# Kernel tuning notes

Measured on AMD Instinct MI355X. Metric: run time of the kernel, lower is better.

Reference implementation:

```python
import jax, jax.numpy as jnp
import numpy as np

DIM, WIDTH = 5, 64
BATCH, N_SAVE = 4096, 64
RTOL, ATOL = 1e-3, 1e-6
SAFETY, FMIN, FMAX = 0.9, 0.2, 10.0
MAX_STEPS, DT0, EPS = 64, 0.1, 1e-6

# Tsit5 (Tsitouras 2011) Butcher tableau
A21 = 0.161
A31, A32 = -0.008480655492356989, 0.335480655492357
A41, A42, A43 = 2.8971530571054935, -6.359448489975075, 4.3622954328695815
A51, A52, A53, A54 = 5.325864828439257, -11.748883564062828, 7.4955393428898365, -0.09249506636175525
A61, A62, A63, A64, A65 = 5.86145544294642, -12.92096931784711, 8.159367898576159, -0.071584973281401, -0.028269050394068383
B1, B2, B3, B4, B5, B6 = 0.09646076681806523, 0.01, 0.4798896504144996, 1.379008574103742, -3.290069515436081, 2.324710524099774
# embedded 4th-order error coefficients (b - bhat)
E1, E2, E3, E4, E5, E6, E7 = (-0.00178001105222577714, -0.0008164344596567469,
    0.007880878010261995, -0.1447110071732629, 0.5823571654525552,
    -0.45808210592918697, 0.015151515151515152)


def _mlp(y, W1, b1, W2, b2, W3, b3, W4, b4):
    # eqx.nn.MLP(5, 5, width 64, depth 3, softplus)
    h = jax.nn.softplus(y @ W1.T + b1)
    h = jax.nn.softplus(h @ W2.T + b2)
    h = jax.nn.softplus(h @ W3.T + b3)
    return h @ W4.T + b4


def _solve_one(y0, t_eval, params):
    f = lambda y: _mlp(y, *params)
    t0, t1 = t_eval[0], t_eval[-1]
    # save points at/before t0 get y0
    ys0 = jnp.where((t_eval <= t0 + EPS)[:, None], y0[None, :], 0.0)

    def body(carry, _):
        t, y, h, ys = carry
        done = t >= t1 - EPS
        hc = jnp.where(done, 0.0, jnp.minimum(h, t1 - t))  # clip last step to t1
        k1 = f(y)
        k2 = f(y + hc * (A21 * k1))
        k3 = f(y + hc * (A31 * k1 + A32 * k2))
        k4 = f(y + hc * (A41 * k1 + A42 * k2 + A43 * k3))
        k5 = f(y + hc * (A51 * k1 + A52 * k2 + A53 * k3 + A54 * k4))
        k6 = f(y + hc * (A61 * k1 + A62 * k2 + A63 * k3 + A64 * k4 + A65 * k5))
        ynew = y + hc * (B1 * k1 + B2 * k2 + B3 * k3 + B4 * k4 + B5 * k5 + B6 * k6)
        k7 = f(ynew)  # FSAL stage, also used for error + interpolation
        err = hc * (E1 * k1 + E2 * k2 + E3 * k3 + E4 * k4 + E5 * k5 + E6 * k6 + E7 * k7)
        scale = ATOL + RTOL * jnp.maximum(jnp.abs(y), jnp.abs(ynew))
        enorm = jnp.sqrt(jnp.mean((err / scale) ** 2))
        enorm_c = jax.lax.stop_gradient(jnp.maximum(enorm, 1e-10))
        accept = enorm <= 1.0
        factor = jnp.clip(SAFETY * enorm_c ** -0.2, FMIN, FMAX)  # I-controller, order 5
        step_ok = accept & ~done
        t_next = jnp.where(step_ok, t + hc, t)
        y_next = jnp.where(step_ok, ynew, y)
        h_next = jnp.where(done, h, hc * factor)
        # cubic Hermite interpolation for save points inside (t, t_next]
        s = ((t_eval - t) / jnp.maximum(hc, 1e-12))[:, None]
        h00 = 2 * s**3 - 3 * s**2 + 1
        h10 = s**3 - 2 * s**2 + s
        h01 = -2 * s**3 + 3 * s**2
        h11 = s**3 - s**2
        yi = h00 * y + h10 * hc * k1 + h01 * ynew + h11 * hc * k7
        mask = (t_eval > t) & (t_eval <= t_next + EPS) & step_ok
        ys = jnp.where(mask[:, None], yi, ys)
        return (t_next, y_next, h_next, ys), None

    h0 = jnp.asarray(DT0, dtype=y0.dtype)
    (_, _, _, ys), _ = jax.lax.scan(body, (t0, y0, h0, ys0), None, length=MAX_STEPS)
    return ys  # [N_SAVE, DIM]


def setup_inputs() -> dict:
    key = jax.random.key(0)
    ks = jax.random.split(key, 9)
    y0 = jax.random.normal(ks[0], (BATCH, DIM), dtype=jnp.float32)
    t_eval = jnp.linspace(0.0, 1.0, N_SAVE, dtype=jnp.float32)

    def lin(k, out_d, in_d):
        lim = 1.0 / np.sqrt(in_d)
        kw, kb = jax.random.split(k)
        W = jax.random.uniform(kw, (out_d, in_d), jnp.float32, -lim, lim)
        b = jax.random.uniform(kb, (out_d,), jnp.float32, -lim, lim)
        return W, b

    W1, b1 = lin(ks[1], WIDTH, DIM)
    W2, b2 = lin(ks[2], WIDTH, WIDTH)
    W3, b3 = lin(ks[3], WIDTH, WIDTH)
    W4, b4 = lin(ks[4], DIM, WIDTH)
    return {"y0": y0, "t_eval": t_eval, "W1": W1, "b1": b1, "W2": W2, "b2": b2,
            "W3": W3, "b3": b3, "W4": W4, "b4": b4}


def reference(y0, t_eval, W1, b1, W2, b2, W3, b3, W4, b4):
    params = (W1, b1, W2, b2, W3, b3, W4, b4)
    return jax.vmap(lambda y: _solve_one(y, t_eval, params))(y0)  # [BATCH, N_SAVE, DIM]
```

## Files before the change

kernel.cpp:

```cpp
#include <hip/hip_runtime.h>
#include <cmath>

namespace {

constexpr int kDim = 5;
constexpr int kSave = 64;
constexpr int kTraj = 16;
constexpr int kThreads = 256;
constexpr int kMaxSteps = 64;
constexpr int HS = 72;
constexpr int SD = 8;

typedef _Float16 half8 __attribute__((ext_vector_type(8)));
typedef float f32x4 __attribute__((ext_vector_type(4)));

__device__ __forceinline__ float softplusf(float x) {
  return fmaxf(x, 0.0f) + __logf(1.0f + __expf(-fabsf(x)));
}

__global__ __launch_bounds__(kThreads, 1)
void node_tsit5_kernel(const float* __restrict__ gy0,
                       const float* __restrict__ gte,
                       const float* __restrict__ gW1, const float* __restrict__ gb1,
                       const float* __restrict__ gW2, const float* __restrict__ gb2,
                       const float* __restrict__ gW3, const float* __restrict__ gb3,
                       const float* __restrict__ gW4, const float* __restrict__ gb4,
                       float* __restrict__ out) {
  const float A21 = 0.161f;
  const float A31 = -0.008480655492356989f, A32 = 0.335480655492357f;
  const float A41 = 2.8971530571054935f, A42 = -6.359448489975075f, A43 = 4.3622954328695815f;
  const float A51 = 5.325864828439257f, A52 = -11.748883564062828f, A53 = 7.4955393428898365f,
              A54 = -0.09249506636175525f;
  const float A61 = 5.86145544294642f, A62 = -12.92096931784711f, A63 = 8.159367898576159f,
              A64 = -0.071584973281401f, A65 = -0.028269050394068383f;
  const float B1 = 0.09646076681806523f, B2 = 0.01f, B3 = 0.4798896504144996f,
              B4 = 1.379008574103742f, B5 = -3.290069515436081f, B6 = 2.324710524099774f;
  const float E1 = -0.00178001105222577714f, E2 = -0.0008164344596567469f,
              E3 = 0.007880878010261995f, E4 = -0.1447110071732629f, E5 = 0.5823571654525552f,
              E6 = -0.45808210592918697f, E7 = 0.015151515151515152f;

  __shared__ __align__(16) _Float16 h0[kTraj * HS], l0[kTraj * HS];
  __shared__ __align__(16) _Float16 h1[kTraj * HS], l1[kTraj * HS];
  __shared__ __align__(16) _Float16 h2[kTraj * HS], l2[kTraj * HS];
  __shared__ float sTe[kSave];
  __shared__ float sY[kTraj * SD], sYN[kTraj * SD], sK1[kTraj * SD], sK7[kTraj * SD];
  __shared__ float ctT[kTraj], ctH[kTraj], ctN[kTraj], ctO[kTraj];

  const int tid = threadIdx.x;
  const int bid = blockIdx.x;
  const int w = tid >> 6;
  const int ln = tid & 63;
  const int quad = ln >> 4;
  const int col = ln & 15;
  const int row0 = quad * 4;
  const int nn = (w << 4) | col;
  const bool cact = col < kDim;
  const bool w0 = (w == 0);

  half8 w2h[2], w3h[2], w4h[2], mfh[2];
  float w1r[kDim];
  #pragma unroll
  for (int d = 0; d < kDim; ++d) w1r[d] = gW1[nn * 5 + d];
  #pragma unroll
  for (int kf = 0; kf < 2; ++kf)
    #pragma unroll
    for (int j = 0; j < 8; ++j) {
      int kk2 = kf * 32 + quad * 8 + j;
      w2h[kf][j] = (_Float16)gW2[nn * 64 + kk2];
      w3h[kf][j] = (_Float16)gW3[nn * 64 + kk2];
      w4h[kf][j] = cact ? (_Float16)gW4[col * 64 + kk2] : (_Float16)0.0f;
      float m = 0.0f;
      #pragma unroll
      for (int d = 0; d < kDim; ++d) m = fmaf(w1r[d], gW4[d * 64 + kk2], m);
      mfh[kf][j] = (_Float16)m;
    }
  const float c1 = gb1[nn], c2 = gb2[nn], c3 = gb3[nn];
  const float c4 = cact ? gb4[col] : 0.0f;
  float cu = 0.0f;
  #pragma unroll
  for (int d = 0; d < kDim; ++d) cu = fmaf(w1r[d], gb4[d], cu);

  if (tid < kSave) sTe[tid] = gte[tid];
  if (tid < kTraj * kDim) {
    int t = tid & 15, d = tid >> 4;
    sY[t * SD + d] = gy0[(size_t)(bid * kTraj + t) * kDim + d];
  }
  {
    float* ob = out + (size_t)bid * kTraj * kSave * kDim;
    for (int idx = tid; idx < kTraj * kSave * kDim; idx += kThreads) ob[idx] = 0.0f;
  }

  f32x4 syr = {0, 0, 0, 0}, synr = {0, 0, 0, 0}, kk[7], uu[7], p_y;
  #pragma unroll
  for (int r = 0; r < 4; ++r) {
    const float* yr = gy0 + (size_t)(bid * kTraj + row0 + r) * kDim;
    float acc = c1;
    #pragma unroll
    for (int d = 0; d < kDim; ++d) acc = fmaf(w1r[d], yr[d], acc);
    p_y[r] = acc;
    if (cact) syr[r] = yr[col];
  }
  __syncthreads();

  const float t0v = sTe[0];
  const float t1v = sTe[kSave - 1];

  {
    int tt = tid & 15, gg = tid >> 4;
    float yv[kDim];
    #pragma unroll
    for (int d = 0; d < kDim; ++d) yv[d] = sY[tt * SD + d];
    #pragma unroll
    for (int q = 0; q < 4; ++q) {
      int n = 4 * gg + q;
      if (sTe[n] <= t0v + 1e-6f) {
        float* op = out + ((size_t)(bid * kTraj + tt) * kSave + n) * kDim;
        #pragma unroll
        for (int d = 0; d < kDim; ++d) op[d] = yv[d];
      }
    }
  }

  auto evalF = [&](f32x4 pre1, f32x4& kOut, f32x4& uOut) {
    #pragma unroll
    for (int r = 0; r < 4; ++r) {
      float s = softplusf(pre1[r]);
      _Float16 hi = (_Float16)s;
      h0[(row0 + r) * HS + nn] = hi;
      l0[(row0 + r) * HS + nn] = (_Float16)(s - (float)hi);
    }
    __syncthreads();
    {
      half8 ah0 = *(const half8*)(h0 + col * HS + quad * 8);
      half8 ah1 = *(const half8*)(h0 + col * HS + 32 + quad * 8);
      half8 al0 = *(const half8*)(l0 + col * HS + quad * 8);
      half8 al1 = *(const half8*)(l0 + col * HS + 32 + quad * 8);
      f32x4 a = {c2, c2, c2, c2};
      f32x4 b = {0, 0, 0, 0};
      a = __builtin_amdgcn_mfma_f32_16x16x32_f16(ah0, w2h[0], a, 0, 0, 0);
      b = __builtin_amdgcn_mfma_f32_16x16x32_f16(al0, w2h[0], b, 0, 0, 0);
      a = __builtin_amdgcn_mfma_f32_16x16x32_f16(ah1, w2h[1], a, 0, 0, 0);
      b = __builtin_amdgcn_mfma_f32_16x16x32_f16(al1, w2h[1], b, 0, 0, 0);
      a += b;
      #pragma unroll
      for (int r = 0; r < 4; ++r) {
        float s = softplusf(a[r]);
        _Float16 hi = (_Float16)s;
        h1[(row0 + r) * HS + nn] = hi;
        l1[(row0 + r) * HS + nn] = (_Float16)(s - (float)hi);
      }
    }
    __syncthreads();
    {
      half8 ah0 = *(const half8*)(h1 + col * HS + quad * 8);
      half8 ah1 = *(const half8*)(h1 + col * HS + 32 + quad * 8);
      half8 al0 = *(const half8*)(l1 + col * HS + quad * 8);
      half8 al1 = *(const half8*)(l1 + col * HS + 32 + quad * 8);
      f32x4 a = {c3, c3, c3, c3};
      f32x4 b = {0, 0, 0, 0};
      a = __builtin_amdgcn_mfma_f32_16x16x32_f16(ah0, w3h[0], a, 0, 0, 0);
      b = __builtin_amdgcn_mfma_f32_16x16x32_f16(al0, w3h[0], b, 0, 0, 0);
      a = __builtin_amdgcn_mfma_f32_16x16x32_f16(ah1, w3h[1], a, 0, 0, 0);
      b = __builtin_amdgcn_mfma_f32_16x16x32_f16(al1, w3h[1], b, 0, 0, 0);
      a += b;
      #pragma unroll
      for (int r = 0; r < 4; ++r) {
        float s = softplusf(a[r]);
        _Float16 hi = (_Float16)s;
        h2[(row0 + r) * HS + nn] = hi;
        l2[(row0 + r) * HS + nn] = (_Float16)(s - (float)hi);
      }
    }
    __syncthreads();
    {
      half8 ah0 = *(const half8*)(h2 + col * HS + quad * 8);
      half8 ah1 = *(const half8*)(h2 + col * HS + 32 + quad * 8);
      half8 al0 = *(const half8*)(l2 + col * HS + quad * 8);
      half8 al1 = *(const half8*)(l2 + col * HS + 32 + quad * 8);
      f32x4 ka = {c4, c4, c4, c4};
      f32x4 kb = {0, 0, 0, 0};
      f32x4 ua = {cu, cu, cu, cu};
      f32x4 ub = {0, 0, 0, 0};
      ka = __builtin_amdgcn_mfma_f32_16x16x32_f16(ah0, w4h[0], ka, 0, 0, 0);
      kb = __builtin_amdgcn_mfma_f32_16x16x32_f16(al0, w4h[0], kb, 0, 0, 0);
      ua = __builtin_amdgcn_mfma_f32_16x16x32_f16(ah0, mfh[0], ua, 0, 0, 0);
      ub = __builtin_amdgcn_mfma_f32_16x16x32_f16(al0, mfh[0], ub, 0, 0, 0);
      ka = __builtin_amdgcn_mfma_f32_16x16x32_f16(ah1, w4h[1], ka, 0, 0, 0);
      kb = __builtin_amdgcn_mfma_f32_16x16x32_f16(al1, w4h[1], kb, 0, 0, 0);
      ua = __builtin_amdgcn_mfma_f32_16x16x32_f16(ah1, mfh[1], ua, 0, 0, 0);
      ub = __builtin_amdgcn_mfma_f32_16x16x32_f16(al1, mfh[1], ub, 0, 0, 0);
      kOut = ka + kb;
      uOut = ua + ub;
    }
  };

  evalF(p_y, kk[0], uu[0]);

  f32x4 tcur = {t0v, t0v, t0v, t0v};
  f32x4 hcur = {0.1f, 0.1f, 0.1f, 0.1f};

  for (int step = 0; step < kMaxSteps; ++step) {
    f32x4 hcs, tOldr;
    bool dnr[4];
    bool all4 = true;
    #pragma unroll
    for (int r = 0; r < 4; ++r) {
      bool d = tcur[r] >= t1v - 1e-6f;
      dnr[r] = d;
      all4 &= d;
      hcs[r] = d ? 0.0f : fminf(hcur[r], t1v - tcur[r]);
      tOldr[r] = tcur[r];
    }
    if (__ballot(all4) == ~0ull) break;

    f32x4 p1;
    #pragma unroll
    for (int r = 0; r < 4; ++r) p1[r] = fmaf(hcs[r], A21 * uu[0][r], p_y[r]);
    evalF(p1, kk[1], uu[1]);

    #pragma unroll
    for (int r = 0; r < 4; ++r)
      p1[r] = fmaf(hcs[r], fmaf(A32, uu[1][r], A31 * uu[0][r]), p_y[r]);
    evalF(p1, kk[2], uu[2]);

    #pragma unroll
    for (int r = 0; r < 4; ++r)
      p1[r] = fmaf(hcs[r], fmaf(A43, uu[2][r], fmaf(A42, uu[1][r], A41 * uu[0][r])), p_y[r]);
    evalF(p1, kk[3], uu[3]);

    #pragma unroll
    for (int r = 0; r < 4; ++r)
      p1[r] = fmaf(hcs[r], fmaf(A54, uu[3][r], fmaf(A53, uu[2][r],
                  fmaf(A52, uu[1][r], A51 * uu[0][r]))), p_y[r]);
    evalF(p1, kk[4], uu[4]);

    #pragma unroll
    for (int r = 0; r < 4; ++r)
      p1[r] = fmaf(hcs[r], fmaf(A65, uu[4][r], fmaf(A64, uu[3][r], fmaf(A63, uu[2][r],
                  fmaf(A62, uu[1][r], A61 * uu[0][r])))), p_y[r]);
    evalF(p1, kk[5], uu[5]);

    f32x4 bu;
    #pragma unroll
    for (int r = 0; r < 4; ++r) {
      bu[r] = fmaf(B6, uu[5][r], fmaf(B5, uu[4][r], fmaf(B4, uu[3][r],
              fmaf(B3, uu[2][r], fmaf(B2, uu[1][r], B1 * uu[0][r])))));
      synr[r] = fmaf(hcs[r], fmaf(B6, kk[5][r], fmaf(B5, kk[4][r], fmaf(B4, kk[3][r],
                 fmaf(B3, kk[2][r], fmaf(B2, kk[1][r], B1 * kk[0][r]))))), syr[r]);
      p1[r] = fmaf(hcs[r], bu[r], p_y[r]);
    }
    if (w0 && cact) {
      #pragma unroll
      for (int r = 0; r < 4; ++r) {
        int o = (row0 + r) * SD + col;
        sY[o] = syr[r];
        sYN[o] = synr[r];
        sK1[o] = kk[0][r];
      }
    }
    evalF(p1, kk[6], uu[6]);

    f32x4 rr2;
    #pragma unroll
    for (int r = 0; r < 4; ++r) {
      float err = hcs[r] * fmaf(E7, kk[6][r], fmaf(E6, kk[5][r], fmaf(E5, kk[4][r],
                  fmaf(E4, kk[3][r], fmaf(E3, kk[2][r], fmaf(E2, kk[1][r], E1 * kk[0][r]))))));
      float sc = fmaf(1e-3f, fmaxf(fabsf(syr[r]), fabsf(synr[r])), 1e-6f);
      float rr = err / sc;
      rr2[r] = cact ? rr * rr : 0.0f;
    }
    #pragma unroll
    for (int m = 1; m < 16; m <<= 1) {
      #pragma unroll
      for (int r = 0; r < 4; ++r) rr2[r] += __shfl_xor(rr2[r], m, 64);
    }

    bool okr[4];
    #pragma unroll
    for (int r = 0; r < 4; ++r) {
      float enorm = sqrtf(rr2[r] / 5.0f);
      float enc = fmaxf(enorm, 1e-10f);
      bool accept = enorm <= 1.0f;
      float factor = fminf(fmaxf(0.9f * __expf(-0.2f * __logf(enc)), 0.2f), 10.0f);
      bool ok = accept && !dnr[r];
      okr[r] = ok;
      tcur[r] = ok ? tcur[r] + hcs[r] : tcur[r];
      hcur[r] = dnr[r] ? hcur[r] : hcs[r] * factor;
    }

    if (w0 && cact) {
      #pragma unroll
      for (int r = 0; r < 4; ++r) sK7[(row0 + r) * SD + col] = kk[6][r];
    }
    if (w0 && col == 0) {
      #pragma unroll
      for (int r = 0; r < 4; ++r) {
        int m2 = row0 + r;
        ctT[m2] = tOldr[r];
        ctH[m2] = hcs[r];
        ctN[m2] = tcur[r];
        ctO[m2] = okr[r] ? 1.0f : 0.0f;
      }
    }
    __syncthreads();

    {
      int tt = tid & 15, gg = tid >> 4;
      if (ctO[tt] != 0.0f) {
        float tOld = ctT[tt], hcv = ctH[tt], tNew = ctN[tt];
        float inv = 1.0f / fmaxf(hcv, 1e-12f);
        float yv[kDim], ynv[kDim], k1v[kDim], k7v[kDim];
        #pragma unroll
        for (int d = 0; d < kDim; ++d) {
          yv[d] = sY[tt * SD + d];
          ynv[d] = sYN[tt * SD + d];
          k1v[d] = hcv * sK1[tt * SD + d];
          k7v[d] = hcv * sK7[tt * SD + d];
        }
        #pragma unroll
        for (int q = 0; q < 4; ++q) {
          int n = 4 * gg + q;
          float te = sTe[n];
          if (te > tOld && te <= tNew + 1e-6f) {
            float sx = (te - tOld) * inv;
            float s2 = sx * sx, s3 = s2 * sx;
            float h00 = 2.f * s3 - 3.f * s2 + 1.f;
            float h10 = s3 - 2.f * s2 + sx;
            float h01 = -2.f * s3 + 3.f * s2;
            float h11 = s3 - s2;
            float* op = out + ((size_t)(bid * kTraj + tt) * kSave + n) * kDim;
            #pragma unroll
            for (int d = 0; d < kDim; ++d)
              op[d] = h00 * yv[d] + h10 * k1v[d] + h01 * ynv[d] + h11 * k7v[d];
          }
        }
      }
    }

    #pragma unroll
    for (int r = 0; r < 4; ++r) {
      if (okr[r]) {
        syr[r] = synr[r];
        kk[0][r] = kk[6][r];
        uu[0][r] = uu[6][r];
        p_y[r] = fmaf(hcs[r], bu[r], p_y[r]);
      }
    }
  }
}

}

extern "C" void kernel_launch(void* const* d_in, const int* in_sizes, int n_in,
                              void* d_out, int out_size, void* d_ws, size_t ws_size,
                              hipStream_t stream) {
  const float* y0 = (const float*)d_in[0];
  const float* te = (const float*)d_in[1];
  const float* W1 = (const float*)d_in[2];
  const float* b1 = (const float*)d_in[3];
  const float* W2 = (const float*)d_in[4];
  const float* b2 = (const float*)d_in[5];
  const float* W3 = (const float*)d_in[6];
  const float* b3 = (const float*)d_in[7];
  const float* W4 = (const float*)d_in[8];
  const float* b4 = (const float*)d_in[9];
  float* out = (float*)d_out;

  const int batch = in_sizes[0] / kDim;
  const int blocks = batch / kTraj;
  hipLaunchKernelGGL(node_tsit5_kernel, dim3(blocks), dim3(kThreads), 0, stream,
                     y0, te, W1, b1, W2, b2, W3, b3, W4, b4, out);
}
```

Measured before the change: 107.8 us.

## Process two interleaved trajectory groups per block to amortize barriers

Each block now integrates two independent groups of 16 trajectories, running the MLP layers for both groups between each shared barrier. Launching half as many blocks means each __syncthreads and its latency is shared by twice the MFMA and softplus work, which gives more independent instructions to overlap. In exchange, register and shared-memory use per block roughly doubles. Fewer blocks (128) may underfill the GPU's compute units, and the early-exit check now waits for the slower of both groups.

```diff
diff --git a/kernel.cpp b/kernel.cpp
--- a/kernel.cpp
+++ b/kernel.cpp
@@ -6,6 +6,7 @@
 constexpr int kDim = 5;
 constexpr int kSave = 64;
 constexpr int kTraj = 16;
+constexpr int kStreams = 2;
 constexpr int kThreads = 256;
 constexpr int kMaxSteps = 64;
 constexpr int HS = 72;
@@ -39,12 +40,14 @@
               E3 = 0.007880878010261995f, E4 = -0.1447110071732629f, E5 = 0.5823571654525552f,
               E6 = -0.45808210592918697f, E7 = 0.015151515151515152f;
 
-  __shared__ __align__(16) _Float16 h0[kTraj * HS], l0[kTraj * HS];
-  __shared__ __align__(16) _Float16 h1[kTraj * HS], l1[kTraj * HS];
-  __shared__ __align__(16) _Float16 h2[kTraj * HS], l2[kTraj * HS];
+  __shared__ __align__(16) _Float16 h0[kStreams][kTraj * HS], l0[kStreams][kTraj * HS];
+  __shared__ __align__(16) _Float16 h1[kStreams][kTraj * HS], l1[kStreams][kTraj * HS];
+  __shared__ __align__(16) _Float16 h2[kStreams][kTraj * HS], l2[kStreams][kTraj * HS];
   __shared__ float sTe[kSave];
-  __shared__ float sY[kTraj * SD], sYN[kTraj * SD], sK1[kTraj * SD], sK7[kTraj * SD];
-  __shared__ float ctT[kTraj], ctH[kTraj], ctN[kTraj], ctO[kTraj];
+  __shared__ float sY[kStreams][kTraj * SD], sYN[kStreams][kTraj * SD];
+  __shared__ float sK1[kStreams][kTraj * SD], sK7[kStreams][kTraj * SD];
+  __shared__ float ctT[kStreams][kTraj], ctH[kStreams][kTraj];
+  __shared__ float ctN[kStreams][kTraj], ctO[kStreams][kTraj];
 
   const int tid = threadIdx.x;
   const int bid = blockIdx.x;
@@ -81,24 +84,30 @@
   for (int d = 0; d < kDim; ++d) cu = fmaf(w1r[d], gb4[d], cu);
 
   if (tid < kSave) sTe[tid] = gte[tid];
-  if (tid < kTraj * kDim) {
-    int t = tid & 15, d = tid >> 4;
-    sY[t * SD + d] = gy0[(size_t)(bid * kTraj + t) * kDim + d];
+  if (tid < kStreams * kTraj * kDim) {
+    int s = tid / (kTraj * kDim), rem = tid % (kTraj * kDim);
+    int t = rem & 15, d = rem >> 4;
+    sY[s][t * SD + d] = gy0[(size_t)(bid * kStreams * kTraj + s * kTraj + t) * kDim + d];
   }
   {
-    float* ob = out + (size_t)bid * kTraj * kSave * kDim;
-    for (int idx = tid; idx < kTraj * kSave * kDim; idx += kThreads) ob[idx] = 0.0f;
-  }
-
-  f32x4 syr = {0, 0, 0, 0}, synr = {0, 0, 0, 0}, kk[7], uu[7], p_y;
+    float* ob = out + (size_t)bid * kStreams * kTraj * kSave * kDim;
+    for (int idx = tid; idx < kStreams * kTraj * kSave * kDim; idx += kThreads)
+      ob[idx] = 0.0f;
+  }
+
+  f32x4 syr[kStreams], synr[kStreams], kkS[kStreams][7], uuS[kStreams][7], p_y[kStreams];
   #pragma unroll
-  for (int r = 0; r < 4; ++r) {
-    const float* yr = gy0 + (size_t)(bid * kTraj + row0 + r) * kDim;
-    float acc = c1;
-    #pragma unroll
-    for (int d = 0; d < kDim; ++d) acc = fmaf(w1r[d], yr[d], acc);
-    p_y[r] = acc;
-    if (cact) syr[r] = yr[col];
+  for (int s = 0; s < kStreams; ++s) {
+    syr[s] = f32x4{0, 0, 0, 0};
+    #pragma unroll
+    for (int r = 0; r < 4; ++r) {
+      const float* yr = gy0 + (size_t)(bid * kStreams * kTraj + s * kTraj + row0 + r) * kDim;
+      float acc = c1;
+      #pragma unroll
+      for (int d = 0; d < kDim; ++d) acc = fmaf(w1r[d], yr[d], acc);
+      p_y[s][r] = acc;
+      if (cact) syr[s][r] = yr[col];
+    }
   }
   __syncthreads();
 
@@ -107,34 +116,42 @@
 
   {
     int tt = tid & 15, gg = tid >> 4;
-    float yv[kDim];
-    #pragma unroll
-    for (int d = 0; d < kDim; ++d) yv[d] = sY[tt * SD + d];
-    #pragma unroll
-    for (int q = 0; q < 4; ++q) {
-      int n = 4 * gg + q;
-      if (sTe[n] <= t0v + 1e-6f) {
-        float* op = out + ((size_t)(bid * kTraj + tt) * kSave + n) * kDim;
-        #pragma unroll
-        for (int d = 0; d < kDim; ++d) op[d] = yv[d];
-      }
-    }
-  }
-
-  auto evalF = [&](f32x4 pre1, f32x4& kOut, f32x4& uOut) {
-    #pragma unroll
-    for (int r = 0; r < 4; ++r) {
-      float s = softplusf(pre1[r]);
-      _Float16 hi = (_Float16)s;
-      h0[(row0 + r) * HS + nn] = hi;
-      l0[(row0 + r) * HS + nn] = (_Float16)(s - (float)hi);
-    }
+    #pragma unroll
+    for (int s = 0; s < kStreams; ++s) {
+      float yv[kDim];
+      #pragma unroll
+      for (int d = 0; d < kDim; ++d) yv[d] = sY[s][tt * SD + d];
+      #pragma unroll
+      for (int q = 0; q < 4; ++q) {
+        int n = 4 * gg + q;
+        if (sTe[n] <= t0v + 1e-6f) {
+          float* op = out +
+              ((size_t)(bid * kStreams * kTraj + s * kTraj + tt) * kSave + n) * kDim;
+          #pragma unroll
+          for (int d = 0; d < kDim; ++d) op[d] = yv[d];
+        }
+      }
+    }
+  }
+
+  auto evalF2 = [&](const f32x4 pre1[kStreams], f32x4 kOut[kStreams],
+                    f32x4 uOut[kStreams]) {
+    #pragma unroll
+    for (int s = 0; s < kStreams; ++s)
+      #pragma unroll
+      for (int r = 0; r < 4; ++r) {
+        float sv = softplusf(pre1[s][r]);
+        _Float16 hi = (_Float16)sv;
+        h0[s][(row0 + r) * HS + nn] = hi;
+        l0[s][(row0 + r) * HS + nn] = (_Float16)(sv - (float)hi);
+      }
     __syncthreads();
-    {
-      half8 ah0 = *(const half8*)(h0 + col * HS + quad * 8);
-      half8 ah1 = *(const half8*)(h0 + col * HS + 32 + quad * 8);
-      half8 al0 = *(const half8*)(l0 + col * HS + quad * 8);
-      half8 al1 = *(const half8*)(l0 + col * HS + 32 + quad * 8);
+    #pragma unroll
+    for (int s = 0; s < kStreams; ++s) {
+      half8 ah0 = *(const half8*)(h0[s] + col * HS + quad * 8);
+      half8 ah1 = *(const half8*)(h0[s] + col * HS + 32 + quad * 8);
+      half8 al0 = *(const half8*)(l0[s] + col * HS + quad * 8);
+      half8 al1 = *(const half8*)(l0[s] + col * HS + 32 + quad * 8);
       f32x4 a = {c2, c2, c2, c2};
       f32x4 b = {0, 0, 0, 0};
       a = __builtin_amdgcn_mfma_f32_16x16x32_f16(ah0, w2h[0], a, 0, 0, 0);
@@ -144,18 +161,19 @@
       a += b;
       #pragma unroll
       for (int r = 0; r < 4; ++r) {
-        float s = softplusf(a[r]);
-        _Float16 hi = (_Float16)s;
-        h1[(row0 + r) * HS + nn] = hi;
-        l1[(row0 + r) * HS + nn] = (_Float16)(s - (float)hi);
+        float sv = softplusf(a[r]);
+        _Float16 hi = (_Float16)sv;
+        h1[s][(row0 + r) * HS + nn] = hi;
+        l1[s][(row0 + r) * HS + nn] = (_Float16)(sv - (float)hi);
       }
     }
     __syncthreads();
-    {
-      half8 ah0 = *(const half8*)(h1 + col * HS + quad * 8);
-      half8 ah1 = *(const half8*)(h1 + col * HS + 32 + quad * 8);
-      half8 al0 = *(const half8*)(l1 + col * HS + quad * 8);
-      half8 al1 = *(const half8*)(l1 + col * HS + 32 + quad * 8);
+    #pragma unroll
+    for (int s = 0; s < kStreams; ++s) {
+      half8 ah0 = *(const half8*)(h1[s] + col * HS + quad * 8);
+      half8 ah1 = *(const half8*)(h1[s] + col * HS + 32 + quad * 8);
+      half8 al0 = *(const half8*)(l1[s] + col * HS + quad * 8);
+      half8 al1 = *(const half8*)(l1[s] + col * HS + 32 + quad * 8);
       f32x4 a = {c3, c3, c3, c3};
       f32x4 b = {0, 0, 0, 0};
       a = __builtin_amdgcn_mfma_f32_16x16x32_f16(ah0, w3h[0], a, 0, 0, 0);
@@ -165,18 +183,19 @@
       a += b;
       #pragma unroll
       for (int r = 0; r < 4; ++r) {
-        float s = softplusf(a[r]);
-        _Float16 hi = (_Float16)s;
-        h2[(row0 + r) * HS + nn] = hi;
-        l2[(row0 + r) * HS + nn] = (_Float16)(s - (float)hi);
+        float sv = softplusf(a[r]);
+        _Float16 hi = (_Float16)sv;
+        h2[s][(row0 + r) * HS + nn] = hi;
+        l2[s][(row0 + r) * HS + nn] = (_Float16)(sv - (float)hi);
       }
     }
     __syncthreads();
-    {
-      half8 ah0 = *(const half8*)(h2 + col * HS + quad * 8);
-      half8 ah1 = *(const half8*)(h2 + col * HS + 32 + quad * 8);
-      half8 al0 = *(const half8*)(l2 + col * HS + quad * 8);
-      half8 al1 = *(const half8*)(l2 + col * HS + 32 + quad * 8);
+    #pragma unroll
+    for (int s = 0; s < kStreams; ++s) {
+      half8 ah0 = *(const half8*)(h2[s] + col * HS + quad * 8);
+      half8 ah1 = *(const half8*)(h2[s] + col * HS + 32 + quad * 8);
+      half8 al0 = *(const half8*)(l2[s] + col * HS + quad * 8);
+      half8 al1 = *(const half8*)(l2[s] + col * HS + 32 + quad * 8);
       f32x4 ka = {c4, c4, c4, c4};
       f32x4 kb = {0, 0, 0, 0};
       f32x4 ua = {cu, cu, cu, cu};
@@ -189,163 +208,218 @@
       kb = __builtin_amdgcn_mfma_f32_16x16x32_f16(al1, w4h[1], kb, 0, 0, 0);
       ua = __builtin_amdgcn_mfma_f32_16x16x32_f16(ah1, mfh[1], ua, 0, 0, 0);
       ub = __builtin_amdgcn_mfma_f32_16x16x32_f16(al1, mfh[1], ub, 0, 0, 0);
-      kOut = ka + kb;
-      uOut = ua + ub;
+      kOut[s] = ka + kb;
+      uOut[s] = ua + ub;
     }
   };
 
-  evalF(p_y, kk[0], uu[0]);
-
-  f32x4 tcur = {t0v, t0v, t0v, t0v};
-  f32x4 hcur = {0.1f, 0.1f, 0.1f, 0.1f};
+  {
+    f32x4 k0[kStreams], u0[kStreams];
+    evalF2(p_y, k0, u0);
+    #pragma unroll
+    for (int s = 0; s < kStreams; ++s) { kkS[s][0] = k0[s]; uuS[s][0] = u0[s]; }
+  }
+
+  f32x4 tcur[kStreams], hcur[kStreams];
+  #pragma unroll
+  for (int s = 0; s < kStreams; ++s) {
+    tcur[s] = f32x4{t0v, t0v, t0v, t0v};
+    hcur[s] = f32x4{0.1f, 0.1f, 0.1f, 0.1f};
+  }
 
   for (int step = 0; step < kMaxSteps; ++step) {
-    f32x4 hcs, tOldr;
-    bool dnr[4];
-    bool all4 = true;
-    #pragma unroll
-    for (int r = 0; r < 4; ++r) {
-      bool d = tcur[r] >= t1v - 1e-6f;
-      dnr[r] = d;
-      all4 &= d;
-      hcs[r] = d ? 0.0f : fminf(hcur[r], t1v - tcur[r]);
-      tOldr[r] = tcur[r];
-    }
-    if (__ballot(all4) == ~0ull) break;
-
-    f32x4 p1;
-    #pragma unroll
-    for (int r = 0; r < 4; ++r) p1[r] = fmaf(hcs[r], A21 * uu[0][r], p_y[r]);
-    evalF(p1, kk[1], uu[1]);
-
-    #pragma unroll
-    for (int r = 0; r < 4; ++r)
-      p1[r] = fmaf(hcs[r], fmaf(A32, uu[1][r], A31 * uu[0][r]), p_y[r]);
-    evalF(p1, kk[2], uu[2]);
-
-    #pragma unroll
-    for (int r = 0; r < 4; ++r)
-      p1[r] = fmaf(hcs[r], fmaf(A43, uu[2][r], fmaf(A42, uu[1][r], A41 * uu[0][r])), p_y[r]);
-    evalF(p1, kk[3], uu[3]);
-
-    #pragma unroll
-    for (int r = 0; r < 4; ++r)
-      p1[r] = fmaf(hcs[r], fmaf(A54, uu[3][r], fmaf(A53, uu[2][r],
-                  fmaf(A52, uu[1][r], A51 * uu[0][r]))), p_y[r]);
-    evalF(p1, kk[4], uu[4]);
-
-    #pragma unroll
-    for (int r = 0; r < 4; ++r)
-      p1[r] = fmaf(hcs[r], fmaf(A65, uu[4][r], fmaf(A64, uu[3][r], fmaf(A63, uu[2][r],
-                  fmaf(A62, uu[1][r], A61 * uu[0][r])))), p_y[r]);
-    evalF(p1, kk[5], uu[5]);
-
-    f32x4 bu;
-    #pragma unroll
-    for (int r = 0; r < 4; ++r) {
-      bu[r] = fmaf(B6, uu[5][r], fmaf(B5, uu[4][r], fmaf(B4, uu[3][r],
-              fmaf(B3, uu[2][r], fmaf(B2, uu[1][r], B1 * uu[0][r])))));
-      synr[r] = fmaf(hcs[r], fmaf(B6, kk[5][r], fmaf(B5, kk[4][r], fmaf(B4, kk[3][r],
-                 fmaf(B3, kk[2][r], fmaf(B2, kk[1][r], B1 * kk[0][r]))))), syr[r]);
-      p1[r] = fmaf(hcs[r], bu[r], p_y[r]);
-    }
+    f32x4 hcs[kStreams], tOldr[kStreams];
+    bool dnr[kStreams][4];
+    bool allA = true;
+    #pragma unroll
+    for (int s = 0; s < kStreams; ++s)
+      #pragma unroll
+      for (int r = 0; r < 4; ++r) {
+        bool d = tcur[s][r] >= t1v - 1e-6f;
+        dnr[s][r] = d;
+        allA &= d;
+        hcs[s][r] = d ? 0.0f : fminf(hcur[s][r], t1v - tcur[s][r]);
+        tOldr[s][r] = tcur[s][r];
+      }
+    if (__ballot(allA) == ~0ull) break;
+
+    f32x4 p1[kStreams], kO[kStreams], uO[kStreams];
+
+    #pragma unroll
+    for (int s = 0; s < kStreams; ++s)
+      #pragma unroll
+      for (int r = 0; r < 4; ++r)
+        p1[s][r] = fmaf(hcs[s][r], A21 * uuS[s][0][r], p_y[s][r]);
+    evalF2(p1, kO, uO);
+    #pragma unroll
+    for (int s = 0; s < kStreams; ++s) { kkS[s][1] = kO[s]; uuS[s][1] = uO[s]; }
+
+    #pragma unroll
+    for (int s = 0; s < kStreams; ++s)
+      #pragma unroll
+      for (int r = 0; r < 4; ++r)
+        p1[s][r] = fmaf(hcs[s][r], fmaf(A32, uuS[s][1][r], A31 * uuS[s][0][r]), p_y[s][r]);
+    evalF2(p1, kO, uO);
+    #pragma unroll
+    for (int s = 0; s < kStreams; ++s) { kkS[s][2] = kO[s]; uuS[s][2] = uO[s]; }
+
+    #pragma unroll
+    for (int s = 0; s < kStreams; ++s)
+      #pragma unroll
+      for (int r = 0; r < 4; ++r)
+        p1[s][r] = fmaf(hcs[s][r], fmaf(A43, uuS[s][2][r],
+                    fmaf(A42, uuS[s][1][r], A41 * uuS[s][0][r])), p_y[s][r]);
+    evalF2(p1, kO, uO);
+    #pragma unroll
+    for (int s = 0; s < kStreams; ++s) { kkS[s][3] = kO[s]; uuS[s][3] = uO[s]; }
+
+    #pragma unroll
+    for (int s = 0; s < kStreams; ++s)
+      #pragma unroll
+      for (int r = 0; r < 4; ++r)
+        p1[s][r] = fmaf(hcs[s][r], fmaf(A54, uuS[s][3][r], fmaf(A53, uuS[s][2][r],
+                    fmaf(A52, uuS[s][1][r], A51 * uuS[s][0][r]))), p_y[s][r]);
+    evalF2(p1, kO, uO);
+    #pragma unroll
+    for (int s = 0; s < kStreams; ++s) { kkS[s][4] = kO[s]; uuS[s][4] = uO[s]; }
+
+    #pragma unroll
+    for (int s = 0; s < kStreams; ++s)
+      #pragma unroll
+      for (int r = 0; r < 4; ++r)
+        p1[s][r] = fmaf(hcs[s][r], fmaf(A65, uuS[s][4][r], fmaf(A64, uuS[s][3][r],
+                    fmaf(A63, uuS[s][2][r], fmaf(A62, uuS[s][1][r],
+                    A61 * uuS[s][0][r])))), p_y[s][r]);
+    evalF2(p1, kO, uO);
+    #pragma unroll
+    for (int s = 0; s < kStreams; ++s) { kkS[s][5] = kO[s]; uuS[s][5] = uO[s]; }
+
+    f32x4 bu[kStreams];
+    #pragma unroll
+    for (int s = 0; s < kStreams; ++s)
+      #pragma unroll
+      for (int r = 0; r < 4; ++r) {
+        bu[s][r] = fmaf(B6, uuS[s][5][r], fmaf(B5, uuS[s][4][r], fmaf(B4, uuS[s][3][r],
+                   fmaf(B3, uuS[s][2][r], fmaf(B2, uuS[s][1][r], B1 * uuS[s][0][r])))));
+        synr[s][r] = fmaf(hcs[s][r], fmaf(B6, kkS[s][5][r], fmaf(B5, kkS[s][4][r],
+                     fmaf(B4, kkS[s][3][r], fmaf(B3, kkS[s][2][r],
+                     fmaf(B2, kkS[s][1][r], B1 * kkS[s][0][r]))))), syr[s][r]);
+        p1[s][r] = fmaf(hcs[s][r], bu[s][r], p_y[s][r]);
+      }
     if (w0 && cact) {
       #pragma unroll
-      for (int r = 0; r < 4; ++r) {
-        int o = (row0 + r) * SD + col;
-        sY[o] = syr[r];
-        sYN[o] = synr[r];
-        sK1[o] = kk[0][r];
-      }
-    }
-    evalF(p1, kk[6], uu[6]);
-
-    f32x4 rr2;
-    #pragma unroll
-    for (int r = 0; r < 4; ++r) {
-      float err = hcs[r] * fmaf(E7, kk[6][r], fmaf(E6, kk[5][r], fmaf(E5, kk[4][r],
-                  fmaf(E4, kk[3][r], fmaf(E3, kk[2][r], fmaf(E2, kk[1][r], E1 * kk[0][r]))))));
-      float sc = fmaf(1e-3f, fmaxf(fabsf(syr[r]), fabsf(synr[r])), 1e-6f);
-      float rr = err / sc;
-      rr2[r] = cact ? rr * rr : 0.0f;
-    }
-    #pragma unroll
-    for (int m = 1; m < 16; m <<= 1) {
-      #pragma unroll
-      for (int r = 0; r < 4; ++r) rr2[r] += __shfl_xor(rr2[r], m, 64);
-    }
-
-    bool okr[4];
-    #pragma unroll
-    for (int r = 0; r < 4; ++r) {
-      float enorm = sqrtf(rr2[r] / 5.0f);
-      float enc = fmaxf(enorm, 1e-10f);
-      bool accept = enorm <= 1.0f;
-      float factor = fminf(fmaxf(0.9f * __expf(-0.2f * __logf(enc)), 0.2f), 10.0f);
-      bool ok = accept && !dnr[r];
-      okr[r] = ok;
-      tcur[r] = ok ? tcur[r] + hcs[r] : tcur[r];
-      hcur[r] = dnr[r] ? hcur[r] : hcs[r] * factor;
+      for (int s = 0; s < kStreams; ++s)
+        #pragma unroll
+        for (int r = 0; r < 4; ++r) {
+          int o = (row0 + r) * SD + col;
+          sY[s][o] = syr[s][r];
+          sYN[s][o] = synr[s][r];
+          sK1[s][o] = kkS[s][0][r];
+        }
+    }
+    evalF2(p1, kO, uO);
+    #pragma unroll
+    for (int s = 0; s < kStreams; ++s) { kkS[s][6] = kO[s]; uuS[s][6] = uO[s]; }
+
+    bool okr[kStreams][4];
+    #pragma unroll
+    for (int s = 0; s < kStreams; ++s) {
+      f32x4 rr2;
+      #pragma unroll
+      for (int r = 0; r < 4; ++r) {
+        float err = hcs[s][r] * fmaf(E7, kkS[s][6][r], fmaf(E6, kkS[s][5][r],
+                    fmaf(E5, kkS[s][4][r], fmaf(E4, kkS[s][3][r], fmaf(E3, kkS[s][2][r],
+                    fmaf(E2, kkS[s][1][r], E1 * kkS[s][0][r]))))));
+        float sc = fmaf(1e-3f, fmaxf(fabsf(syr[s][r]), fabsf(synr[s][r])), 1e-6f);
+        float rr = err / sc;
+        rr2[r] = cact ? rr * rr : 0.0f;
+      }
+      #pragma unroll
+      for (int m = 1; m < 16; m <<= 1) {
+        #pragma unroll
+        for (int r = 0; r < 4; ++r) rr2[r] += __shfl_xor(rr2[r], m, 64);
+      }
+      #pragma unroll
+      for (int r = 0; r < 4; ++r) {
+        float enorm = sqrtf(rr2[r] / 5.0f);
+        float enc = fmaxf(enorm, 1e-10f);
+        bool accept = enorm <= 1.0f;
+        float factor = fminf(fmaxf(0.9f * __expf(-0.2f * __logf(enc)), 0.2f), 10.0f);
+        bool ok = accept && !dnr[s][r];
+        okr[s][r] = ok;
+        tcur[s][r] = ok ? tcur[s][r] + hcs[s][r] : tcur[s][r];
+        hcur[s][r] = dnr[s][r] ? hcur[s][r] : hcs[s][r] * factor;
+      }
     }
 
     if (w0 && cact) {
       #pragma unroll
-      for (int r = 0; r < 4; ++r) sK7[(row0 + r) * SD + col] = kk[6][r];
+      for (int s = 0; s < kStreams; ++s)
+        #pragma unroll
+        for (int r = 0; r < 4; ++r) sK7[s][(row0 + r) * SD + col] = kkS[s][6][r];
     }
     if (w0 && col == 0) {
       #pragma unroll
-      for (int r = 0; r < 4; ++r) {
-        int m2 = row0 + r;
-        ctT[m2] = tOldr[r];
-        ctH[m2] = hcs[r];
-        ctN[m2] = tcur[r];
-        ctO[m2] = okr[r] ? 1.0f : 0.0f;
-      }
+      for (int s = 0; s < kStreams; ++s)
+        #pragma unroll
+        for (int r = 0; r < 4; ++r) {
+          int m2 = row0 + r;
+          ctT[s][m2] = tOldr[s][r];
+          ctH[s][m2] = hcs[s][r];
+          ctN[s][m2] = tcur[s][r];
+          ctO[s][m2] = okr[s][r] ? 1.0f : 0.0f;
+        }
     }
     __syncthreads();
 
     {
       int tt = tid & 15, gg = tid >> 4;
-      if (ctO[tt] != 0.0f) {
-        float tOld = ctT[tt], hcv = ctH[tt], tNew = ctN[tt];
-        float inv = 1.0f / fmaxf(hcv, 1e-12f);
-        float yv[kDim], ynv[kDim], k1v[kDim], k7v[kDim];
-        #pragma unroll
-        for (int d = 0; d < kDim; ++d) {
-          yv[d] = sY[tt * SD + d];
-          ynv[d] = sYN[tt * SD + d];
-          k1v[d] = hcv * sK1[tt * SD + d];
-          k7v[d] = hcv * sK7[tt * SD + d];
-        }
-        #pragma unroll
-        for (int q = 0; q < 4; ++q) {
-          int n = 4 * gg + q;
-          float te = sTe[n];
-          if (te > tOld && te <= tNew + 1e-6f) {
-            float sx = (te - tOld) * inv;
-            float s2 = sx * sx, s3 = s2 * sx;
-            float h00 = 2.f * s3 - 3.f * s2 + 1.f;
-            float h10 = s3 - 2.f * s2 + sx;
-            float h01 = -2.f * s3 + 3.f * s2;
-            float h11 = s3 - s2;
-            float* op = out + ((size_t)(bid * kTraj + tt) * kSave + n) * kDim;
-            #pragma unroll
-            for (int d = 0; d < kDim; ++d)
-              op[d] = h00 * yv[d] + h10 * k1v[d] + h01 * ynv[d] + h11 * k7v[d];
+      #pragma unroll
+      for (int s = 0; s < kStreams; ++s) {
+        if (ctO[s][tt] != 0.0f) {
+          float tOld = ctT[s][tt], hcv = ctH[s][tt], tNew = ctN[s][tt];
+          float inv = 1.0f / fmaxf(hcv, 1e-12f);
+          float yv[kDim], ynv[kDim], k1v[kDim], k7v[kDim];
+          #pragma unroll
+          for (int d = 0; d < kDim; ++d) {
+            yv[d] = sY[s][tt * SD + d];
+            ynv[d] = sYN[s][tt * SD + d];
+            k1v[d] = hcv * sK1[s][tt * SD + d];
+            k7v[d] = hcv * sK7[s][tt * SD + d];
+          }
+          #pragma unroll
+          for (int q = 0; q < 4; ++q) {
+            int n = 4 * gg + q;
+            float te = sTe[n];
+            if (te > tOld && te <= tNew + 1e-6f) {
+              float sx = (te - tOld) * inv;
+              float s2 = sx * sx, s3 = s2 * sx;
+              float h00 = 2.f * s3 - 3.f * s2 + 1.f;
+              float h10 = s3 - 2.f * s2 + sx;
+              float h01 = -2.f * s3 + 3.f * s2;
+              float h11 = s3 - s2;
+              float* op = out +
+                  ((size_t)(bid * kStreams * kTraj + s * kTraj + tt) * kSave + n) * kDim;
+              #pragma unroll
+              for (int d = 0; d < kDim; ++d)
+                op[d] = h00 * yv[d] + h10 * k1v[d] + h01 * ynv[d] + h11 * k7v[d];
+            }
           }
         }
       }
     }
 
     #pragma unroll
-    for (int r = 0; r < 4; ++r) {
-      if (okr[r]) {
-        syr[r] = synr[r];
-        kk[0][r] = kk[6][r];
-        uu[0][r] = uu[6][r];
-        p_y[r] = fmaf(hcs[r], bu[r], p_y[r]);
-      }
-    }
+    for (int s = 0; s < kStreams; ++s)
+      #pragma unroll
+      for (int r = 0; r < 4; ++r) {
+        if (okr[s][r]) {
+          syr[s][r] = synr[s][r];
+          kkS[s][0][r] = kkS[s][6][r];
+          uuS[s][0][r] = uuS[s][6][r];
+          p_y[s][r] = fmaf(hcs[s][r], bu[s][r], p_y[s][r]);
+        }
+      }
   }
 }
 
@@ -367,7 +441,7 @@
   float* out = (float*)d_out;
 
   const int batch = in_sizes[0] / kDim;
-  const int blocks = batch / kTraj;
+  const int blocks = batch / (kTraj * kStreams);
   hipLaunchKernelGGL(node_tsit5_kernel, dim3(blocks), dim3(kThreads), 0, stream,
                      y0, te, W1, b1, W2, b2, W3, b3, W4, b4, out);
 }
```

Measured after the change: 128.5 us. +19.2%, slower.
